# Kernel optimization log

Measured on AMD Instinct MI355X. Metric: run time of the kernel, lower is better.

The kernel has to match this reference:

```python
import jax, jax.numpy as jnp
import numpy as np

# Mamba-2 config (from MambaBackbone defaults)
D_MODEL = 512
D_STATE = 64
D_CONV = 4
EXPAND = 2
HEADDIM = 64
CHUNK = 256
D_INNER = EXPAND * D_MODEL            # 1024
NHEADS = D_INNER // HEADDIM           # 16
CONV_DIM = D_INNER + 2 * D_STATE      # 1152 (ngroups=1)
D_IN_PROJ = 2 * D_INNER + 2 * D_STATE + NHEADS  # 2192


def setup_inputs() -> dict:
    key = jax.random.key(0)
    ks = jax.random.split(key, 8)
    B, T = 4, 4096
    x = jax.random.normal(ks[0], (B, T, D_MODEL), dtype=jnp.float32)
    W_in = jax.random.normal(ks[1], (D_IN_PROJ, D_MODEL), dtype=jnp.float32) * 0.02
    conv_w = jax.random.normal(ks[2], (CONV_DIM, D_CONV), dtype=jnp.float32) * 0.2
    conv_b = jnp.zeros((CONV_DIM,), jnp.float32)
    # dt_bias initialized so softplus(dt_bias) ~ Uniform-log[1e-3, 1e-1] (mamba2 init)
    dt0 = jnp.exp(jax.random.uniform(ks[3], (NHEADS,)) * (np.log(0.1) - np.log(0.001)) + np.log(0.001))
    dt_bias = dt0 + jnp.log(-jnp.expm1(-dt0))
    A_log = jnp.log(jnp.arange(1, NHEADS + 1, dtype=jnp.float32))  # A = -exp(A_log) in [-16,-1]
    D = jnp.ones((NHEADS,), jnp.float32)
    norm_w = jnp.ones((D_INNER,), jnp.float32)
    W_out = jax.random.normal(ks[4], (D_MODEL, D_INNER), dtype=jnp.float32) * 0.02
    return dict(x=x, W_in=W_in, conv_w=conv_w, conv_b=conv_b, dt_bias=dt_bias,
                A_log=A_log, D=D, norm_w=norm_w, W_out=W_out)


def segsum(a):
    """a: (..., l) -> (..., l, l) with [i,j] = sum_{j<k<=i} a[..,k]; -inf above diag."""
    l = a.shape[-1]
    cs = jnp.cumsum(a, axis=-1)
    ss = cs[..., :, None] - cs[..., None, :]
    mask = jnp.tril(jnp.ones((l, l), dtype=bool))
    return jnp.where(mask, ss, -jnp.inf)


def reference(x, W_in, conv_w, conv_b, dt_bias, A_log, D, norm_w, W_out):
    Bb, T, _ = x.shape
    # input projection -> [z | xBC | dt]
    zxbcdt = x @ W_in.T                                    # (B,T,2192)
    z = zxbcdt[..., :D_INNER]
    xBC = zxbcdt[..., D_INNER:D_INNER + CONV_DIM]
    dt = zxbcdt[..., -NHEADS:]
    # causal depthwise conv1d (kernel D_CONV) + SiLU
    xp = jnp.pad(xBC, ((0, 0), (D_CONV - 1, 0), (0, 0)))
    conv = sum(xp[:, k:k + T, :] * conv_w[:, k] for k in range(D_CONV)) + conv_b
    xBC = jax.nn.silu(conv)
    xs = xBC[..., :D_INNER].reshape(Bb, T, NHEADS, HEADDIM)  # (B,T,H,P)
    Bm = xBC[..., D_INNER:D_INNER + D_STATE]                 # (B,T,N)  ngroups=1
    Cm = xBC[..., D_INNER + D_STATE:]                        # (B,T,N)
    dt = jax.nn.softplus(dt + dt_bias)                       # (B,T,H)
    A = -jnp.exp(A_log)                                      # (H,)
    # ---- chunked SSD (Mamba-2) ----
    nc = T // CHUNK
    Ad = (dt * A).reshape(Bb, nc, CHUNK, NHEADS).transpose(0, 3, 1, 2)   # (b,h,c,l) log-decay
    x_dt = (xs * dt[..., None]).reshape(Bb, nc, CHUNK, NHEADS, HEADDIM)  # (b,c,l,h,p)
    Bc = Bm.reshape(Bb, nc, CHUNK, D_STATE)                              # (b,c,l,n)
    Cc = Cm.reshape(Bb, nc, CHUNK, D_STATE)
    A_cs = jnp.cumsum(Ad, axis=-1)                                       # (b,h,c,l)
    L = jnp.exp(segsum(Ad))                                              # (b,h,c,l,l)
    # intra-chunk (diagonal blocks)
    Y_diag = jnp.einsum('bcln,bcsn,bhcls,bcshp->bclhp', Cc, Bc, L, x_dt)
    # per-chunk end states
    decay_states = jnp.exp(A_cs[..., -1:] - A_cs)                        # (b,h,c,l)
    states = jnp.einsum('bcln,bhcl,bclhp->cbhpn', Bc, decay_states, x_dt)
    chunk_decay = jnp.exp(A_cs[..., -1]).transpose(2, 0, 1)              # (c,b,h)
    def step(h, inp):
        dec, st = inp
        return dec[..., None, None] * h + st, h                          # emit state BEFORE chunk
    h0 = jnp.zeros_like(states[0])
    _, prev = jax.lax.scan(step, h0, (chunk_decay, states))              # (c,b,h,p,n)
    # inter-chunk contribution
    Y_off = jnp.einsum('bcln,cbhpn,bhcl->bclhp', Cc, prev, jnp.exp(A_cs))
    y = (Y_diag + Y_off).reshape(Bb, T, NHEADS, HEADDIM) + D[None, None, :, None] * xs
    y = y.reshape(Bb, T, D_INNER)
    # gated RMSNorm: rmsnorm(y * silu(z)) * w   (norm_before_gate=False)
    yz = y * jax.nn.silu(z)
    out = yz * jax.lax.rsqrt(jnp.mean(yz * yz, axis=-1, keepdims=True) + 1e-5) * norm_w
    return out @ W_out.T
```

## Files before the change

kernel.cpp:

```cpp
#include <hip/hip_runtime.h>
#include <hip/hip_bf16.h>
#include <cstdint>

typedef unsigned int  uint;
typedef unsigned short ushort;
using bf16 = __hip_bfloat16;

#define B_     4
#define T_     4096
#define DM     512
#define DI     1024
#define DSTATE 64
#define HD     64
#define NH     16
#define NC     16
#define CHK    256
#define CONVD  1152
#define DPROJ  2192

using f32x4 = __attribute__((ext_vector_type(4))) float;
using s16x8 = __attribute__((ext_vector_type(8))) short;

#define MFMA16(a, b, c) __builtin_amdgcn_mfma_f32_16x16x32_bf16((a), (b), (c), 0, 0, 0)

__device__ inline void unpack8(const uint4 v, float* f) {
  const uint w[4] = {v.x, v.y, v.z, v.w};
#pragma unroll
  for (int i = 0; i < 4; ++i) {
    f[2*i]   = __uint_as_float(w[i] << 16);
    f[2*i+1] = __uint_as_float(w[i] & 0xffff0000u);
  }
}
__device__ inline void unpack4(const uint2 v, float* f) {
  f[0] = __uint_as_float(v.x << 16); f[1] = __uint_as_float(v.x & 0xffff0000u);
  f[2] = __uint_as_float(v.y << 16); f[3] = __uint_as_float(v.y & 0xffff0000u);
}
__device__ inline ushort bfbits(float a) {
  bf16 h = __float2bfloat16(a);
  return *reinterpret_cast<ushort*>(&h);
}
__device__ inline uint pack2(float a, float b) {
  return (uint)bfbits(a) | ((uint)bfbits(b) << 16);
}
__device__ inline uint4 pack8(const float* f) {
  uint4 v;
  v.x = pack2(f[0], f[1]); v.y = pack2(f[2], f[3]);
  v.z = pack2(f[4], f[5]); v.w = pack2(f[6], f[7]);
  return v;
}

__device__ __forceinline__ void gl_lds16(const void* g, void* l) {
  __builtin_amdgcn_global_load_lds(
      (const __attribute__((address_space(1))) unsigned int*)g,
      (__attribute__((address_space(3))) unsigned int*)l, 16, 0, 0);
}

__global__ __launch_bounds__(256)
void cast_bf16(const float* __restrict__ in, short* __restrict__ out, int n8) {
  const int i = blockIdx.x * 256 + threadIdx.x;
  if (i >= n8) return;
  float f[8];
  float4 a = *reinterpret_cast<const float4*>(&in[(size_t)i * 8]);
  float4 b = *reinterpret_cast<const float4*>(&in[(size_t)i * 8 + 4]);
  f[0]=a.x; f[1]=a.y; f[2]=a.z; f[3]=a.w; f[4]=b.x; f[5]=b.y; f[6]=b.z; f[7]=b.w;
  *reinterpret_cast<uint4*>(&out[(size_t)i * 8]) = pack8(f);
}

template<int EPI>
__global__ __launch_bounds__(256)
void gemm_mfma(const short* __restrict__ A, const short* __restrict__ Bw,
               int K, int N, int nbx, float* __restrict__ Cout,
               short* __restrict__ z, short* __restrict__ xbc,
               float* __restrict__ dtr) {
  __shared__ __align__(16) char smem[(EPI == 1) ? 34816 : 32768];
  short* As = reinterpret_cast<short*>(smem);
  short* Bs = As + 128 * 64;
  const int tid  = threadIdx.x;
  const int lane = tid & 63, w = tid >> 6;
  const int hi = lane >> 4, lo = lane & 15;
  const int lx = lo & 7;
  const int wr = w >> 1, wc = w & 1;

  const int cpx = gridDim.x >> 3;
  const int swz = (blockIdx.x & 7) * cpx + (blockIdx.x >> 3);
  const int bm = (swz / nbx) * 128, bn = (swz % nbx) * 128;

  f32x4 acc[4][4] = {};

  const int srow = lane >> 3;
  const int scol = ((lane & 7) ^ srow) * 8;

  for (int k0 = 0; k0 < K; k0 += 64) {
#pragma unroll
    for (int i = 0; i < 4; ++i) {
      const int seg = w * 4 + i;
      const int row = seg * 8 + srow;
      gl_lds16(&A[(size_t)(bm + row) * K + k0 + scol], &As[seg * 512]);
      const int brow = (bn + row < N) ? (bn + row) : (N - 1);
      gl_lds16(&Bw[(size_t)brow * K + k0 + scol], &Bs[seg * 512]);
    }
    __syncthreads();
#pragma unroll
    for (int kb = 0; kb < 2; ++kb) {
      s16x8 af[4], bf[4];
#pragma unroll
      for (int t = 0; t < 4; ++t) {
        const int gg = ((kb * 4 + hi) ^ lx) * 8;
        af[t] = *reinterpret_cast<const s16x8*>(&As[(wr*64 + t*16 + lo) * 64 + gg]);
        bf[t] = *reinterpret_cast<const s16x8*>(&Bs[(wc*64 + t*16 + lo) * 64 + gg]);
      }
#pragma unroll
      for (int lt = 0; lt < 4; ++lt)
#pragma unroll
        for (int nt = 0; nt < 4; ++nt)
          acc[lt][nt] = MFMA16(af[lt], bf[nt], acc[lt][nt]);
    }
    __syncthreads();
  }

  if (EPI == 0) {
#pragma unroll
    for (int lt = 0; lt < 4; ++lt)
#pragma unroll
      for (int nt = 0; nt < 4; ++nt) {
        const int cg = bn + wc * 64 + nt * 16 + lo;
#pragma unroll
        for (int r = 0; r < 4; ++r) {
          const int rg = bm + wr * 64 + lt * 16 + hi * 4 + r;
          Cout[(size_t)rg * DM + cg] = acc[lt][nt][r];
        }
      }
  } else {
    if (bn + 128 > DI + CONVD) {
#pragma unroll
      for (int lt = 0; lt < 4; ++lt)
#pragma unroll
        for (int nt = 0; nt < 4; ++nt) {
          const int cg = bn + wc * 64 + nt * 16 + lo;
          if (cg >= DI + CONVD && cg < DPROJ) {
#pragma unroll
            for (int r = 0; r < 4; ++r) {
              const int rg = bm + wr * 64 + lt * 16 + hi * 4 + r;
              dtr[(size_t)rg * NH + (cg - DI - CONVD)] = acc[lt][nt][r];
            }
          }
        }
    }
    ushort (*tile)[136] = reinterpret_cast<ushort(*)[136]>(smem);
    __syncthreads();
#pragma unroll
    for (int lt = 0; lt < 4; ++lt)
#pragma unroll
      for (int nt = 0; nt < 4; ++nt) {
        const int cl = wc * 64 + nt * 16 + lo;
#pragma unroll
        for (int r = 0; r < 4; ++r)
          tile[wr * 64 + lt * 16 + hi * 4 + r][cl] = bfbits(acc[lt][nt][r]);
      }
    __syncthreads();
#pragma unroll
    for (int it = 0; it < 8; ++it) {
      const int unit = it * 256 + tid;
      const int row = unit >> 4;
      const int c8  = (unit & 15) << 3;
      const int cg  = bn + c8;
      const int rg  = bm + row;
      if (cg >= DI + CONVD) continue;
      uint4 v = *reinterpret_cast<const uint4*>(&tile[row][c8]);
      if (cg < DI)
        *reinterpret_cast<uint4*>(&reinterpret_cast<ushort*>(z)[(size_t)rg * DI + cg]) = v;
      else
        *reinterpret_cast<uint4*>(&reinterpret_cast<ushort*>(xbc)[(size_t)rg * CONVD + (cg - DI)]) = v;
    }
  }
}

__global__ __launch_bounds__(256)
void conv_silu(const short* __restrict__ xbc, const float* __restrict__ cw,
               const float* __restrict__ cb, short* __restrict__ xc) {
  const int idx = blockIdx.x * 256 + threadIdx.x;
  const int cp = idx % 576;
  const int tb = idx / 576;
  const int ch = cp * 2;
  const int b  = tb >> 9;
  const int t0 = (tb & 511) << 3;
  const long base = ((long)b * T_ + t0) * CONVD + ch;

  const float4 wa = *reinterpret_cast<const float4*>(&cw[ch * 4]);
  const float4 wb = *reinterpret_cast<const float4*>(&cw[ch * 4 + 4]);
  const float ba = cb[ch], bb = cb[ch + 1];

  float va[11], vb[11];
#pragma unroll
  for (int i = 0; i < 11; ++i) {
    const int t = t0 - 3 + i;
    if (t >= 0) {
      const uint u = *reinterpret_cast<const uint*>(&xbc[base + (long)(i - 3) * CONVD]);
      va[i] = __uint_as_float(u << 16);
      vb[i] = __uint_as_float(u & 0xffff0000u);
    } else { va[i] = 0.f; vb[i] = 0.f; }
  }
#pragma unroll
  for (int j = 0; j < 8; ++j) {
    float sa = ba + va[j]*wa.x + va[j+1]*wa.y + va[j+2]*wa.z + va[j+3]*wa.w;
    float sb = bb + vb[j]*wb.x + vb[j+1]*wb.y + vb[j+2]*wb.z + vb[j+3]*wb.w;
    sa = sa / (1.f + __expf(-sa));
    sb = sb / (1.f + __expf(-sb));
    *reinterpret_cast<uint*>(&xc[base + (long)j * CONVD]) = pack2(sa, sb);
  }
}

__global__ __launch_bounds__(256)
void dt_softplus(const float* __restrict__ dtr, const float* __restrict__ dt_bias,
                 float* __restrict__ dtp) {
  const int idx = blockIdx.x * 256 + threadIdx.x;
  const int h = idx & 15;
  const float v = dtr[idx] + dt_bias[h];
  dtp[idx] = (v > 20.f) ? v : log1pf(expf(v));
}

__global__ __launch_bounds__(256, 2)
void ssd_chunk_mfma(const short* __restrict__ xc, const float* __restrict__ dtp,
                    const float* __restrict__ A_log, const float* __restrict__ Dvec,
                    float* __restrict__ acs_g, float* __restrict__ states,
                    short* __restrict__ y) {
  const int bid = blockIdx.x;
  const int h = bid >> 6, b = (bid >> 4) & 3, c = bid & 15;
  const int tid = threadIdx.x;
  const int lane = tid & 63, w = tid >> 6;
  const int hi = lane >> 4, lo = lane & 15;

  __shared__ __align__(16) float acs[CHK];
  __shared__ float wsum[4];
  __shared__ __align__(16) short Bsm[64 * 64];
  __shared__ __align__(16) uint Btm2[64 * 36];
  __shared__ __align__(16) uint Xtm2[64 * 36];
  __shared__ __align__(16) uint Xdm2[64 * 36];
  __shared__ __align__(16) short Pb[4][16][72];

  const size_t row0 = (size_t)b * T_ + (size_t)c * CHK;

  const float Ah = -expf(A_log[h]);
  float v = dtp[(row0 + tid) * NH + h] * Ah;
#pragma unroll
  for (int off = 1; off < 64; off <<= 1) {
    const float u = __shfl_up(v, off);
    if (lane >= off) v += u;
  }
  if (lane == 63) wsum[w] = v;
  __syncthreads();
  float pre = 0.f;
#pragma unroll
  for (int ww = 0; ww < 4; ++ww) if (ww < w) pre += wsum[ww];
  v += pre;
  acs[tid] = v;
  acs_g[(((size_t)b * NH + h) * NC + c) * CHK + tid] = v;
  __syncthreads();
  const float acs_last = acs[CHK - 1];

  s16x8 creg[4][2];
#pragma unroll
  for (int lt = 0; lt < 4; ++lt)
#pragma unroll
    for (int kb = 0; kb < 2; ++kb)
      creg[lt][kb] = *reinterpret_cast<const s16x8*>(
          &xc[(row0 + w*64 + lt*16 + lo) * CONVD + DI + DSTATE + kb*32 + hi*8]);

  f32x4 yacc[4][4] = {};
  f32x4 stacc[4]   = {};

  const int sp2 = tid & 31;
  const int g   = tid >> 5;
  const int srow8 = lane >> 3;
  const int gsrc  = ((lane & 7) ^ srow8) * 8;

  for (int ss = 0; ss < 4; ++ss) {
    const int s0 = ss * 64;
#pragma unroll
    for (int i = 0; i < 2; ++i) {
      const int seg = w * 2 + i;
      gl_lds16(&xc[(row0 + s0 + seg * 8 + srow8) * (size_t)CONVD + DI + gsrc],
               &Bsm[seg * 512]);
    }
    {
      const int se = s0 + 2 * sp2;
      const size_t re = (row0 + se) * (size_t)CONVD;
      const size_t ro = re + CONVD;
      uint4 bqe = *reinterpret_cast<const uint4*>(&xc[re + DI + g*8]);
      uint4 bqo = *reinterpret_cast<const uint4*>(&xc[ro + DI + g*8]);
      uint4 xqe = *reinterpret_cast<const uint4*>(&xc[re + h*HD + g*8]);
      uint4 xqo = *reinterpret_cast<const uint4*>(&xc[ro + h*HD + g*8]);
      const float de_ = dtp[(row0 + se) * NH + h];
      const float do_ = dtp[(row0 + se + 1) * NH + h];
      const float ee = __expf(acs_last - acs[se]);
      const float eo = __expf(acs_last - acs[se + 1]);
      const ushort* beu = reinterpret_cast<const ushort*>(&bqe);
      const ushort* bou = reinterpret_cast<const ushort*>(&bqo);
      float fe[8], fo[8];
      unpack8(xqe, fe); unpack8(xqo, fo);
#pragma unroll
      for (int j = 0; j < 8; ++j) {
        const int cidx = (g * 8 + j) * 36 + sp2;
        Btm2[cidx] = (uint)beu[j] | ((uint)bou[j] << 16);
        const float te = fe[j] * de_, to = fo[j] * do_;
        Xtm2[cidx] = pack2(te, to);
        Xdm2[cidx] = pack2(te * ee, to * eo);
      }
    }
    __syncthreads();

#pragma unroll
    for (int kb = 0; kb < 2; ++kb) {
      s16x8 xdf = *reinterpret_cast<const s16x8*>(&Xdm2[(w*16 + lo)*36 + kb*16 + hi*4]);
#pragma unroll
      for (int nt = 0; nt < 4; ++nt) {
        s16x8 btf = *reinterpret_cast<const s16x8*>(&Btm2[(nt*16 + lo)*36 + kb*16 + hi*4]);
        stacc[nt] = MFMA16(xdf, btf, stacc[nt]);
      }
    }

    if (ss <= w) {
#pragma unroll
      for (int lt = 0; lt < 4; ++lt) {
        f32x4 sacc[4] = {};
#pragma unroll
        for (int st = 0; st < 4; ++st) {
          const int r = st * 16 + lo;
          s16x8 b0 = *reinterpret_cast<const s16x8*>(&Bsm[r*64 + ((0*4 + hi) ^ (lo & 7)) * 8]);
          s16x8 b1 = *reinterpret_cast<const s16x8*>(&Bsm[r*64 + ((1*4 + hi) ^ (lo & 7)) * 8]);
          sacc[st] = MFMA16(b0, creg[lt][0], sacc[st]);
          sacc[st] = MFMA16(b1, creg[lt][1], sacc[st]);
        }
        const int lg = w*64 + lt*16 + lo;
        const float al = acs[lg];
#pragma unroll
        for (int st = 0; st < 4; ++st) {
          float p4[4];
#pragma unroll
          for (int r = 0; r < 4; ++r) {
            const int s = s0 + st*16 + hi*4 + r;
            const float wgt = (s <= lg) ? __expf(al - acs[s]) : 0.f;
            p4[r] = sacc[st][r] * wgt;
          }
          uint2 pk; pk.x = pack2(p4[0], p4[1]); pk.y = pack2(p4[2], p4[3]);
          *reinterpret_cast<uint2*>(&Pb[w][lo][st*16 + hi*4]) = pk;
        }
#pragma unroll
        for (int kb = 0; kb < 2; ++kb) {
          s16x8 pfr = *reinterpret_cast<const s16x8*>(&Pb[w][lo][kb*32 + hi*8]);
#pragma unroll
          for (int pt = 0; pt < 4; ++pt) {
            s16x8 xfr = *reinterpret_cast<const s16x8*>(&Xtm2[(pt*16 + lo)*36 + kb*16 + hi*4]);
            yacc[pt][lt] = MFMA16(xfr, pfr, yacc[pt][lt]);
          }
        }
      }
    }
    __syncthreads();
  }

  const float Dh = Dvec[h];
#pragma unroll
  for (int lt = 0; lt < 4; ++lt) {
    const int l = w*64 + lt*16 + lo;
    ushort* yrow = reinterpret_cast<ushort*>(&y[(row0 + l) * DI + h * HD]);
    const short* xrow = &xc[(row0 + l) * CONVD + h * HD];
#pragma unroll
    for (int pt = 0; pt < 4; ++pt) {
      const int p0 = pt*16 + hi*4;
      uint2 xb2 = *reinterpret_cast<const uint2*>(&xrow[p0]);
      float xf[4]; unpack4(xb2, xf);
      float o[4];
#pragma unroll
      for (int r = 0; r < 4; ++r) o[r] = yacc[pt][lt][r] + Dh * xf[r];
      uint2 pk; pk.x = pack2(o[0], o[1]); pk.y = pack2(o[2], o[3]);
      *reinterpret_cast<uint2*>(&yrow[p0]) = pk;
    }
  }
  {
    const size_t sbase = (((size_t)c * B_ + b) * NH + h) * (HD * DSTATE);
#pragma unroll
    for (int nt = 0; nt < 4; ++nt) {
      const int n = nt*16 + lo;
#pragma unroll
      for (int r = 0; r < 4; ++r) {
        const int p = w*16 + hi*4 + r;
        states[sbase + (size_t)p * DSTATE + n] = stacc[nt][r];
      }
    }
  }
}

__global__ __launch_bounds__(256)
void chunk_scan(const float* __restrict__ acs_g, const float* __restrict__ st,
                short* __restrict__ pv) {
  const int idx = blockIdx.x * 256 + threadIdx.x;
  const int pn = idx & 4095;
  const int h  = (idx >> 12) & 15;
  const int b  = idx >> 16;
  float hst = 0.f;
#pragma unroll
  for (int c = 0; c < NC; ++c) {
    const size_t o = (((size_t)c * B_ + b) * NH + h) * 4096 + pn;
    reinterpret_cast<ushort*>(pv)[o] = bfbits(hst);
    const float dec = __expf(acs_g[(((size_t)b * NH + h) * NC + c) * CHK + CHK - 1]);
    hst = dec * hst + st[o];
  }
}

__global__ __launch_bounds__(256)
void yoff_mfma(const short* __restrict__ xc, const float* __restrict__ acs_g,
               const short* __restrict__ pv, short* __restrict__ y) {
  const int bid = blockIdx.x;
  const int h = bid >> 6, b = (bid >> 4) & 3, c = bid & 15;
  const int tid = threadIdx.x;
  const int lane = tid & 63, w = tid >> 6;
  const int hi = lane >> 4, lo = lane & 15;
  const size_t row0 = (size_t)b * T_ + (size_t)c * CHK;
  const float* ac = &acs_g[(((size_t)b * NH + h) * NC + c) * CHK];
  const short* pvb = &pv[(((size_t)c * B_ + b) * NH + h) * 4096];

  s16x8 creg[4][2];
#pragma unroll
  for (int lt = 0; lt < 4; ++lt)
#pragma unroll
    for (int kb = 0; kb < 2; ++kb)
      creg[lt][kb] = *reinterpret_cast<const s16x8*>(
          &xc[(row0 + w*64 + lt*16 + lo) * CONVD + DI + DSTATE + kb*32 + hi*8]);

  f32x4 acc[4][4] = {};
#pragma unroll
  for (int kb = 0; kb < 2; ++kb) {
    s16x8 pf[4];
#pragma unroll
    for (int pt = 0; pt < 4; ++pt)
      pf[pt] = *reinterpret_cast<const s16x8*>(&pvb[(pt*16 + lo) * DSTATE + kb*32 + hi*8]);
#pragma unroll
    for (int pt = 0; pt < 4; ++pt)
#pragma unroll
      for (int lt = 0; lt < 4; ++lt)
        acc[pt][lt] = MFMA16(pf[pt], creg[lt][kb], acc[pt][lt]);
  }
#pragma unroll
  for (int lt = 0; lt < 4; ++lt) {
    const int l = w*64 + lt*16 + lo;
    const float el = __expf(ac[l]);
    ushort* yrow = reinterpret_cast<ushort*>(&y[(row0 + l) * DI + h * HD]);
#pragma unroll
    for (int pt = 0; pt < 4; ++pt) {
      const int p0 = pt*16 + hi*4;
      uint2 cur = *reinterpret_cast<const uint2*>(&yrow[p0]);
      float f[4]; unpack4(cur, f);
#pragma unroll
      for (int r = 0; r < 4; ++r) f[r] += el * acc[pt][lt][r];
      uint2 pk; pk.x = pack2(f[0], f[1]); pk.y = pack2(f[2], f[3]);
      *reinterpret_cast<uint2*>(&yrow[p0]) = pk;
    }
  }
}

__global__ __launch_bounds__(256)
void gate_rmsnorm(const short* __restrict__ z, const float* __restrict__ norm_w,
                  short* __restrict__ y) {
  const int row = blockIdx.x;
  const int tid = threadIdx.x;
  const short* zrow = &z[(size_t)row * DI];
  short* yrow = &y[(size_t)row * DI];
  uint2 yb = *reinterpret_cast<const uint2*>(&yrow[tid * 4]);
  uint2 zb = *reinterpret_cast<const uint2*>(&zrow[tid * 4]);
  float yv[4], zv[4];
  unpack4(yb, yv); unpack4(zb, zv);
  float tq[4];
  float ss = 0.f;
#pragma unroll
  for (int j = 0; j < 4; ++j) {
    const float sil = zv[j] / (1.f + __expf(-zv[j]));
    tq[j] = yv[j] * sil;
    ss += tq[j] * tq[j];
  }
#pragma unroll
  for (int off = 32; off >= 1; off >>= 1) ss += __shfl_down(ss, off);
  __shared__ float red[4];
  if ((tid & 63) == 0) red[tid >> 6] = ss;
  __syncthreads();
  const float tot = red[0] + red[1] + red[2] + red[3];
  const float r = rsqrtf(tot * (1.f / (float)DI) + 1e-5f);
  float4 wv = *reinterpret_cast<const float4*>(&norm_w[tid * 4]);
  uint2 ob;
  ob.x = pack2(tq[0] * r * wv.x, tq[1] * r * wv.y);
  ob.y = pack2(tq[2] * r * wv.z, tq[3] * r * wv.w);
  *reinterpret_cast<uint2*>(&yrow[tid * 4]) = ob;
}

extern "C" void kernel_launch(void* const* d_in, const int* in_sizes, int n_in,
                              void* d_out, int out_size, void* d_ws, size_t ws_size,
                              hipStream_t stream) {
  const float* x       = (const float*)d_in[0];
  const float* W_in    = (const float*)d_in[1];
  const float* conv_w  = (const float*)d_in[2];
  const float* conv_b  = (const float*)d_in[3];
  const float* dt_bias = (const float*)d_in[4];
  const float* A_log   = (const float*)d_in[5];
  const float* Dv      = (const float*)d_in[6];
  const float* norm_w  = (const float*)d_in[7];
  const float* W_out   = (const float*)d_in[8];
  float* out = (float*)d_out;

  char* w0 = (char*)d_ws;
  short* z    = (short*)(w0);
  short* xbc  = (short*)(w0 + 33554432ULL);
  short* xc   = (short*)(w0 + 71303168ULL);
  short* wob  = (short*)(w0 + 109051904ULL);
  float* dtr  = (float*)(w0 + 110100480ULL);
  float* dtp  = (float*)(w0 + 111149056ULL);
  float* acs  = (float*)(w0 + 112197632ULL);
  float* st   = (float*)(w0 + 113246208ULL);
  short* pv   = (short*)(w0 + 130023424ULL);
  short* xb   = xc;
  short* wb   = (short*)st;
  short* y    = xbc;

  const int M = B_ * T_;

  cast_bf16<<<(M * DM / 8 + 255) / 256, 256, 0, stream>>>(x, xb, M * DM / 8);
  cast_bf16<<<(DPROJ * DM / 8 + 255) / 256, 256, 0, stream>>>(W_in, wb, DPROJ * DM / 8);
  cast_bf16<<<(DM * DI / 8 + 255) / 256, 256, 0, stream>>>(W_out, wob, DM * DI / 8);

  const int nbx_in = (DPROJ + 127) / 128;
  gemm_mfma<1><<<nbx_in * (M / 128), 256, 0, stream>>>(
      xb, wb, DM, DPROJ, nbx_in, nullptr, z, xbc, dtr);
  conv_silu<<<(M / 8) * 576 / 256, 256, 0, stream>>>(xbc, conv_w, conv_b, xc);
  dt_softplus<<<(M * NH) / 256, 256, 0, stream>>>(dtr, dt_bias, dtp);
  ssd_chunk_mfma<<<B_ * NC * NH, 256, 0, stream>>>(xc, dtp, A_log, Dv, acs, st, y);
  chunk_scan<<<(B_ * NH * HD * DSTATE) / 256, 256, 0, stream>>>(acs, st, pv);
  yoff_mfma<<<B_ * NC * NH, 256, 0, stream>>>(xc, acs, pv, y);
  gate_rmsnorm<<<M, 256, 0, stream>>>(z, norm_w, y);
  gemm_mfma<0><<<(DM / 128) * (M / 128), 256, 0, stream>>>(
      y, wob, DI, DM, DM / 128, out, nullptr, nullptr, nullptr);
}
```

Before: 221.4 us.

## Split SSD into states and output kernels, fuse dt softplus and Y_off

```diff
diff --git a/kernel.cpp b/kernel.cpp
--- a/kernel.cpp
+++ b/kernel.cpp
@@ -71,7 +71,7 @@
 void gemm_mfma(const short* __restrict__ A, const short* __restrict__ Bw,
                int K, int N, int nbx, float* __restrict__ Cout,
                short* __restrict__ z, short* __restrict__ xbc,
-               float* __restrict__ dtr) {
+               float* __restrict__ dtp, const float* __restrict__ dt_bias) {
   __shared__ __align__(16) char smem[(EPI == 1) ? 34816 : 32768];
   short* As = reinterpret_cast<short*>(smem);
   short* Bs = As + 128 * 64;
@@ -138,10 +138,13 @@
         for (int nt = 0; nt < 4; ++nt) {
           const int cg = bn + wc * 64 + nt * 16 + lo;
           if (cg >= DI + CONVD && cg < DPROJ) {
+            const float bia = dt_bias[cg - DI - CONVD];
 #pragma unroll
             for (int r = 0; r < 4; ++r) {
               const int rg = bm + wr * 64 + lt * 16 + hi * 4 + r;
-              dtr[(size_t)rg * NH + (cg - DI - CONVD)] = acc[lt][nt][r];
+              const float v = acc[lt][nt][r] + bia;
+              dtp[(size_t)rg * NH + (cg - DI - CONVD)] =
+                  (v > 20.f) ? v : log1pf(expf(v));
             }
           }
         }
@@ -211,19 +214,9 @@
 }
 
 __global__ __launch_bounds__(256)
-void dt_softplus(const float* __restrict__ dtr, const float* __restrict__ dt_bias,
-                 float* __restrict__ dtp) {
-  const int idx = blockIdx.x * 256 + threadIdx.x;
-  const int h = idx & 15;
-  const float v = dtr[idx] + dt_bias[h];
-  dtp[idx] = (v > 20.f) ? v : log1pf(expf(v));
-}
-
-__global__ __launch_bounds__(256, 2)
-void ssd_chunk_mfma(const short* __restrict__ xc, const float* __restrict__ dtp,
-                    const float* __restrict__ A_log, const float* __restrict__ Dvec,
-                    float* __restrict__ acs_g, float* __restrict__ states,
-                    short* __restrict__ y) {
+void ssd_states(const short* __restrict__ xc, const float* __restrict__ dtp,
+                const float* __restrict__ A_log,
+                float* __restrict__ acs_g, float* __restrict__ states) {
   const int bid = blockIdx.x;
   const int h = bid >> 6, b = (bid >> 4) & 3, c = bid & 15;
   const int tid = threadIdx.x;
@@ -232,11 +225,8 @@
 
   __shared__ __align__(16) float acs[CHK];
   __shared__ float wsum[4];
-  __shared__ __align__(16) short Bsm[64 * 64];
   __shared__ __align__(16) uint Btm2[64 * 36];
-  __shared__ __align__(16) uint Xtm2[64 * 36];
   __shared__ __align__(16) uint Xdm2[64 * 36];
-  __shared__ __align__(16) short Pb[4][16][72];
 
   const size_t row0 = (size_t)b * T_ + (size_t)c * CHK;
 
@@ -258,30 +248,12 @@
   __syncthreads();
   const float acs_last = acs[CHK - 1];
 
-  s16x8 creg[4][2];
-#pragma unroll
-  for (int lt = 0; lt < 4; ++lt)
-#pragma unroll
-    for (int kb = 0; kb < 2; ++kb)
-      creg[lt][kb] = *reinterpret_cast<const s16x8*>(
-          &xc[(row0 + w*64 + lt*16 + lo) * CONVD + DI + DSTATE + kb*32 + hi*8]);
-
-  f32x4 yacc[4][4] = {};
-  f32x4 stacc[4]   = {};
-
+  f32x4 stacc[4] = {};
   const int sp2 = tid & 31;
   const int g   = tid >> 5;
-  const int srow8 = lane >> 3;
-  const int gsrc  = ((lane & 7) ^ srow8) * 8;
 
   for (int ss = 0; ss < 4; ++ss) {
     const int s0 = ss * 64;
-#pragma unroll
-    for (int i = 0; i < 2; ++i) {
-      const int seg = w * 2 + i;
-      gl_lds16(&xc[(row0 + s0 + seg * 8 + srow8) * (size_t)CONVD + DI + gsrc],
-               &Bsm[seg * 512]);
-    }
     {
       const int se = s0 + 2 * sp2;
       const size_t re = (row0 + se) * (size_t)CONVD;
@@ -290,10 +262,8 @@
       uint4 bqo = *reinterpret_cast<const uint4*>(&xc[ro + DI + g*8]);
       uint4 xqe = *reinterpret_cast<const uint4*>(&xc[re + h*HD + g*8]);
       uint4 xqo = *reinterpret_cast<const uint4*>(&xc[ro + h*HD + g*8]);
-      const float de_ = dtp[(row0 + se) * NH + h];
-      const float do_ = dtp[(row0 + se + 1) * NH + h];
-      const float ee = __expf(acs_last - acs[se]);
-      const float eo = __expf(acs_last - acs[se + 1]);
+      const float de_ = dtp[(row0 + se) * NH + h] * __expf(acs_last - acs[se]);
+      const float do_ = dtp[(row0 + se + 1) * NH + h] * __expf(acs_last - acs[se + 1]);
       const ushort* beu = reinterpret_cast<const ushort*>(&bqe);
       const ushort* bou = reinterpret_cast<const ushort*>(&bqo);
       float fe[8], fo[8];
@@ -302,13 +272,10 @@
       for (int j = 0; j < 8; ++j) {
         const int cidx = (g * 8 + j) * 36 + sp2;
         Btm2[cidx] = (uint)beu[j] | ((uint)bou[j] << 16);
-        const float te = fe[j] * de_, to = fo[j] * do_;
-        Xtm2[cidx] = pack2(te, to);
-        Xdm2[cidx] = pack2(te * ee, to * eo);
+        Xdm2[cidx] = pack2(fe[j] * de_, fo[j] * do_);
       }
     }
     __syncthreads();
-
 #pragma unroll
     for (int kb = 0; kb < 2; ++kb) {
       s16x8 xdf = *reinterpret_cast<const s16x8*>(&Xdm2[(w*16 + lo)*36 + kb*16 + hi*4]);
@@ -318,6 +285,122 @@
         stacc[nt] = MFMA16(xdf, btf, stacc[nt]);
       }
     }
+    __syncthreads();
+  }
+
+  const size_t sbase = (((size_t)c * B_ + b) * NH + h) * (HD * DSTATE);
+#pragma unroll
+  for (int nt = 0; nt < 4; ++nt) {
+    const int n = nt*16 + lo;
+#pragma unroll
+    for (int r = 0; r < 4; ++r) {
+      const int p = w*16 + hi*4 + r;
+      states[sbase + (size_t)p * DSTATE + n] = stacc[nt][r];
+    }
+  }
+}
+
+__global__ __launch_bounds__(256)
+void chunk_scan(const float* __restrict__ acs_g, const float* __restrict__ st,
+                short* __restrict__ pv) {
+  const int idx = blockIdx.x * 256 + threadIdx.x;
+  const int pn = idx & 4095;
+  const int h  = (idx >> 12) & 15;
+  const int b  = idx >> 16;
+  float hst = 0.f;
+#pragma unroll
+  for (int c = 0; c < NC; ++c) {
+    const size_t o = (((size_t)c * B_ + b) * NH + h) * 4096 + pn;
+    reinterpret_cast<ushort*>(pv)[o] = bfbits(hst);
+    const float dec = __expf(acs_g[(((size_t)b * NH + h) * NC + c) * CHK + CHK - 1]);
+    hst = dec * hst + st[o];
+  }
+}
+
+__global__ __launch_bounds__(256, 2)
+void ssd_y(const short* __restrict__ xc, const float* __restrict__ dtp,
+           const float* __restrict__ acs_g, const short* __restrict__ pv,
+           const float* __restrict__ Dvec, short* __restrict__ y) {
+  const int bid = blockIdx.x;
+  const int h = bid >> 6, b = (bid >> 4) & 3, c = bid & 15;
+  const int tid = threadIdx.x;
+  const int lane = tid & 63, w = tid >> 6;
+  const int hi = lane >> 4, lo = lane & 15;
+
+  __shared__ __align__(16) float acs[CHK];
+  __shared__ __align__(16) float ds[CHK];
+  __shared__ __align__(16) short Bsm[64 * 64];
+  __shared__ __align__(16) uint Xtm2[64 * 36];
+  __shared__ __align__(16) short Pb[4][16][72];
+
+  const size_t row0 = (size_t)b * T_ + (size_t)c * CHK;
+  const float* acg = &acs_g[(((size_t)b * NH + h) * NC + c) * CHK];
+
+  acs[tid] = acg[tid];
+  __syncthreads();
+  ds[tid] = (tid > 0) ? __expf(acs[tid] - acs[tid - 1]) : 1.f;
+
+  s16x8 creg[4][2];
+#pragma unroll
+  for (int lt = 0; lt < 4; ++lt)
+#pragma unroll
+    for (int kb = 0; kb < 2; ++kb)
+      creg[lt][kb] = *reinterpret_cast<const s16x8*>(
+          &xc[(row0 + w*64 + lt*16 + lo) * CONVD + DI + DSTATE + kb*32 + hi*8]);
+
+  f32x4 yacc[4][4] = {};
+  {
+    const short* pvb = &pv[(((size_t)c * B_ + b) * NH + h) * 4096];
+#pragma unroll
+    for (int kb = 0; kb < 2; ++kb) {
+      s16x8 pf[4];
+#pragma unroll
+      for (int pt = 0; pt < 4; ++pt)
+        pf[pt] = *reinterpret_cast<const s16x8*>(&pvb[(pt*16 + lo) * DSTATE + kb*32 + hi*8]);
+#pragma unroll
+      for (int pt = 0; pt < 4; ++pt)
+#pragma unroll
+        for (int lt = 0; lt < 4; ++lt)
+          yacc[pt][lt] = MFMA16(pf[pt], creg[lt][kb], yacc[pt][lt]);
+    }
+  }
+  __syncthreads();
+#pragma unroll
+  for (int lt = 0; lt < 4; ++lt) {
+    const float el = __expf(acs[w*64 + lt*16 + lo]);
+#pragma unroll
+    for (int pt = 0; pt < 4; ++pt)
+#pragma unroll
+      for (int r = 0; r < 4; ++r) yacc[pt][lt][r] *= el;
+  }
+
+  const int sp2 = tid & 31;
+  const int g   = tid >> 5;
+  const int srow8 = lane >> 3;
+  const int gsrc  = ((lane & 7) ^ srow8) * 8;
+
+  for (int ss = 0; ss < 4; ++ss) {
+    const int s0 = ss * 64;
+#pragma unroll
+    for (int i = 0; i < 2; ++i) {
+      const int seg = w * 2 + i;
+      gl_lds16(&xc[(row0 + s0 + seg * 8 + srow8) * (size_t)CONVD + DI + gsrc],
+               &Bsm[seg * 512]);
+    }
+    {
+      const int se = s0 + 2 * sp2;
+      const size_t re = (row0 + se) * (size_t)CONVD;
+      uint4 xqe = *reinterpret_cast<const uint4*>(&xc[re + h*HD + g*8]);
+      uint4 xqo = *reinterpret_cast<const uint4*>(&xc[re + CONVD + h*HD + g*8]);
+      const float de_ = dtp[(row0 + se) * NH + h];
+      const float do_ = dtp[(row0 + se + 1) * NH + h];
+      float fe[8], fo[8];
+      unpack8(xqe, fe); unpack8(xqo, fo);
+#pragma unroll
+      for (int j = 0; j < 8; ++j)
+        Xtm2[(g * 8 + j) * 36 + sp2] = pack2(fe[j] * de_, fo[j] * do_);
+    }
+    __syncthreads();
 
     if (ss <= w) {
 #pragma unroll
@@ -335,13 +418,16 @@
         const float al = acs[lg];
 #pragma unroll
         for (int st = 0; st < 4; ++st) {
+          const int sb = s0 + st*16 + hi*4;
+          float wv[4];
+          wv[3] = __expf(al - acs[sb + 3]);
+          wv[2] = wv[3] * ds[sb + 3];
+          wv[1] = wv[2] * ds[sb + 2];
+          wv[0] = wv[1] * ds[sb + 1];
           float p4[4];
 #pragma unroll
-          for (int r = 0; r < 4; ++r) {
-            const int s = s0 + st*16 + hi*4 + r;
-            const float wgt = (s <= lg) ? __expf(al - acs[s]) : 0.f;
-            p4[r] = sacc[st][r] * wgt;
-          }
+          for (int r = 0; r < 4; ++r)
+            p4[r] = (sb + r <= lg) ? sacc[st][r] * wv[r] : 0.f;
           uint2 pk; pk.x = pack2(p4[0], p4[1]); pk.y = pack2(p4[2], p4[3]);
           *reinterpret_cast<uint2*>(&Pb[w][lo][st*16 + hi*4]) = pk;
         }
@@ -374,86 +460,6 @@
 #pragma unroll
       for (int r = 0; r < 4; ++r) o[r] = yacc[pt][lt][r] + Dh * xf[r];
       uint2 pk; pk.x = pack2(o[0], o[1]); pk.y = pack2(o[2], o[3]);
-      *reinterpret_cast<uint2*>(&yrow[p0]) = pk;
-    }
-  }
-  {
-    const size_t sbase = (((size_t)c * B_ + b) * NH + h) * (HD * DSTATE);
-#pragma unroll
-    for (int nt = 0; nt < 4; ++nt) {
-      const int n = nt*16 + lo;
-#pragma unroll
-      for (int r = 0; r < 4; ++r) {
-        const int p = w*16 + hi*4 + r;
-        states[sbase + (size_t)p * DSTATE + n] = stacc[nt][r];
-      }
-    }
-  }
-}
-
-__global__ __launch_bounds__(256)
-void chunk_scan(const float* __restrict__ acs_g, const float* __restrict__ st,
-                short* __restrict__ pv) {
-  const int idx = blockIdx.x * 256 + threadIdx.x;
-  const int pn = idx & 4095;
-  const int h  = (idx >> 12) & 15;
-  const int b  = idx >> 16;
-  float hst = 0.f;
-#pragma unroll
-  for (int c = 0; c < NC; ++c) {
-    const size_t o = (((size_t)c * B_ + b) * NH + h) * 4096 + pn;
-    reinterpret_cast<ushort*>(pv)[o] = bfbits(hst);
-    const float dec = __expf(acs_g[(((size_t)b * NH + h) * NC + c) * CHK + CHK - 1]);
-    hst = dec * hst + st[o];
-  }
-}
-
-__global__ __launch_bounds__(256)
-void yoff_mfma(const short* __restrict__ xc, const float* __restrict__ acs_g,
-               const short* __restrict__ pv, short* __restrict__ y) {
-  const int bid = blockIdx.x;
-  const int h = bid >> 6, b = (bid >> 4) & 3, c = bid & 15;
-  const int tid = threadIdx.x;
-  const int lane = tid & 63, w = tid >> 6;
-  const int hi = lane >> 4, lo = lane & 15;
-  const size_t row0 = (size_t)b * T_ + (size_t)c * CHK;
-  const float* ac = &acs_g[(((size_t)b * NH + h) * NC + c) * CHK];
-  const short* pvb = &pv[(((size_t)c * B_ + b) * NH + h) * 4096];
-
-  s16x8 creg[4][2];
-#pragma unroll
-  for (int lt = 0; lt < 4; ++lt)
-#pragma unroll
-    for (int kb = 0; kb < 2; ++kb)
-      creg[lt][kb] = *reinterpret_cast<const s16x8*>(
-          &xc[(row0 + w*64 + lt*16 + lo) * CONVD + DI + DSTATE + kb*32 + hi*8]);
-
-  f32x4 acc[4][4] = {};
-#pragma unroll
-  for (int kb = 0; kb < 2; ++kb) {
-    s16x8 pf[4];
-#pragma unroll
-    for (int pt = 0; pt < 4; ++pt)
-      pf[pt] = *reinterpret_cast<const s16x8*>(&pvb[(pt*16 + lo) * DSTATE + kb*32 + hi*8]);
-#pragma unroll
-    for (int pt = 0; pt < 4; ++pt)
-#pragma unroll
-      for (int lt = 0; lt < 4; ++lt)
-        acc[pt][lt] = MFMA16(pf[pt], creg[lt][kb], acc[pt][lt]);
-  }
-#pragma unroll
-  for (int lt = 0; lt < 4; ++lt) {
-    const int l = w*64 + lt*16 + lo;
-    const float el = __expf(ac[l]);
-    ushort* yrow = reinterpret_cast<ushort*>(&y[(row0 + l) * DI + h * HD]);
-#pragma unroll
-    for (int pt = 0; pt < 4; ++pt) {
-      const int p0 = pt*16 + hi*4;
-      uint2 cur = *reinterpret_cast<const uint2*>(&yrow[p0]);
-      float f[4]; unpack4(cur, f);
-#pragma unroll
-      for (int r = 0; r < 4; ++r) f[r] += el * acc[pt][lt][r];
-      uint2 pk; pk.x = pack2(f[0], f[1]); pk.y = pack2(f[2], f[3]);
       *reinterpret_cast<uint2*>(&yrow[p0]) = pk;
     }
   }
@@ -511,7 +517,6 @@
   short* xbc  = (short*)(w0 + 33554432ULL);
   short* xc   = (short*)(w0 + 71303168ULL);
   short* wob  = (short*)(w0 + 109051904ULL);
-  float* dtr  = (float*)(w0 + 110100480ULL);
   float* dtp  = (float*)(w0 + 111149056ULL);
   float* acs  = (float*)(w0 + 112197632ULL);
   float* st   = (float*)(w0 + 113246208ULL);
@@ -528,13 +533,12 @@
 
   const int nbx_in = (DPROJ + 127) / 128;
   gemm_mfma<1><<<nbx_in * (M / 128), 256, 0, stream>>>(
-      xb, wb, DM, DPROJ, nbx_in, nullptr, z, xbc, dtr);
+      xb, wb, DM, DPROJ, nbx_in, nullptr, z, xbc, dtp, dt_bias);
   conv_silu<<<(M / 8) * 576 / 256, 256, 0, stream>>>(xbc, conv_w, conv_b, xc);
-  dt_softplus<<<(M * NH) / 256, 256, 0, stream>>>(dtr, dt_bias, dtp);
-  ssd_chunk_mfma<<<B_ * NC * NH, 256, 0, stream>>>(xc, dtp, A_log, Dv, acs, st, y);
+  ssd_states<<<B_ * NC * NH, 256, 0, stream>>>(xc, dtp, A_log, acs, st);
   chunk_scan<<<(B_ * NH * HD * DSTATE) / 256, 256, 0, stream>>>(acs, st, pv);
-  yoff_mfma<<<B_ * NC * NH, 256, 0, stream>>>(xc, acs, pv, y);
+  ssd_y<<<B_ * NC * NH, 256, 0, stream>>>(xc, dtp, acs, pv, Dv, y);
   gate_rmsnorm<<<M, 256, 0, stream>>>(z, norm_w, y);
   gemm_mfma<0><<<(DM / 128) * (M / 128), 256, 0, stream>>>(
-      y, wob, DI, DM, DM / 128, out, nullptr, nullptr, nullptr);
-}
+      y, wob, DI, DM, DM / 128, out, nullptr, nullptr, nullptr, nullptr);
+}
```

Result: faster. 206.7 us (-6.7%).
